# Performance work log

Hardware: AMD Instinct MI355X
Metric: run time of the kernel (lower is better)

Reference implementation:

```python
import jax, jax.numpy as jnp
import numpy as np

SPATIAL, CROP = 128, 256


def definePsf(N, M, slope):
    # standard LCT psf (O'Toole et al.), as used in Wenzheng Chen's torch port
    x = (np.arange(2 * N, dtype=np.float32) / (2 * N - 1)) * 2 - 1
    z = (np.arange(2 * M, dtype=np.float32) / (2 * M - 1)) * 2
    gy, gx = np.meshgrid(x, x)
    psf = np.abs(((4 * slope) ** 2) * (gx[None] ** 2 + gy[None] ** 2) - z[:, None, None])
    psf = (psf == psf.min(axis=0, keepdims=True)).astype(np.float32)
    psf = psf / psf[:, N, N].sum()
    psf = psf / np.linalg.norm(psf.ravel())
    psf = np.roll(psf, N, axis=1)
    psf = np.roll(psf, N, axis=2)
    return psf


def resamplingOperator(M):
    row = M ** 2
    x = np.arange(row, dtype=np.float64) + 1
    mtx = np.zeros((row, M), dtype=np.float64)
    mtx[np.arange(row), (np.ceil(np.sqrt(x)) - 1).astype(np.int64)] = 1
    mtx = mtx / x[:, None]
    mtxi = mtx.T.copy()
    for _ in range(int(np.log2(M))):
        mtx = 0.5 * (mtx[0::2] + mtx[1::2])
        mtxi = 0.5 * (mtxi[:, 0::2] + mtxi[:, 1::2])
    return mtx.astype(np.float32), mtxi.astype(np.float32)


def setup_inputs() -> dict:
    key = jax.random.key(0)
    k1, k2 = jax.random.split(key)
    B, D, T, H = 1, 1, CROP, SPATIAL
    feture = jax.random.uniform(k1, (B, D, T, H, H), dtype=jnp.float32)

    c = 3e8
    bin_len = 0.01
    wall_size = 2.0
    trange = CROP * c * (bin_len / c)
    slope = (wall_size / 2.0) / trange
    psf = definePsf(SPATIAL, CROP, slope)
    fpsf = np.fft.fftn(psf)
    snr = 0.1
    invpsf = np.conjugate(fpsf) / (1.0 / snr + np.real(fpsf) ** 2 + np.imag(fpsf) ** 2)

    mtx, mtxi = resamplingOperator(CROP)
    gridz = (np.arange(CROP, dtype=np.float32) / (CROP - 1)).reshape(1, CROP, 1, 1)
    learnable_w = 0.01 * jax.random.normal(k2, (2,) + psf.shape, dtype=jnp.float32)

    return dict(
        feture=feture,
        gridz=jnp.asarray(gridz),
        mtx=jnp.asarray(mtx),
        mtxi=jnp.asarray(mtxi),
        invpsf_real=jnp.asarray(np.real(invpsf).astype(np.float32)),
        invpsf_imag=jnp.asarray(np.imag(invpsf).astype(np.float32)),
        learnable_w=learnable_w,
    )


def reference(feture, gridz, mtx, mtxi, invpsf_real, invpsf_imag, learnable_w):
    B, D, T, H, W = feture.shape
    # diffuse falloff compensation: * z^4
    data = feture.reshape(B * D, T, H, W) * gridz ** 4
    # temporal resampling GEMM: [M,T] @ [BD,T,HW]
    tmp = jnp.einsum('mt,bthw->bmhw', mtx, data)
    # zero-pad to 2T x 2H x 2W
    pad = jnp.zeros((B * D, 2 * T, 2 * H, 2 * W), jnp.float32).at[:, :T, :H, :W].set(tmp)
    # full (non-onesided) complex 3D FFT of real data
    fre = jnp.fft.fftn(pad, axes=(1, 2, 3))
    # learned + fixed inverse filter in frequency domain
    wf = (learnable_w[0] + invpsf_real) + 1j * (learnable_w[1] + invpsf_imag)
    vol = jnp.fft.ifftn(fre * wf, axes=(1, 2, 3)).real[:, :T, :H, :W]
    # inverse temporal resampling GEMM
    out = jnp.einsum('mt,bthw->bmhw', mtxi, vol)
    return out.reshape(B, D, T, H, W)
```

## Files before the change

### kernel.cpp

```cpp
#include <hip/hip_runtime.h>
#include <math.h>

#define TC 256
#define HC 128
#define Z2 512
#define Y2 256
#define X2 256
#define HW 16384
#define LSTR256 260
#define LSTR512 519
#define WPAD 132
#define KZS 257

__device__ __forceinline__ float2 cadd(float2 a, float2 b){ return make_float2(a.x+b.x, a.y+b.y); }
__device__ __forceinline__ float2 csub(float2 a, float2 b){ return make_float2(a.x-b.x, a.y-b.y); }

template<int SGN>
__device__ __forceinline__ float2 cmul_tw(float2 z, float2 w){
  float wy = (SGN < 0) ? w.y : -w.y;
  return make_float2(z.x*w.x - z.y*wy, z.x*wy + z.y*w.x);
}
template<int SGN>
__device__ __forceinline__ float2 mul_pmi(float2 t){
  return (SGN < 0) ? make_float2(t.y, -t.x) : make_float2(-t.y, t.x);
}

template<int SGN>
__device__ __forceinline__ void dft16(float2 r[16], const float2* __restrict__ tw){
  float2 u[16];
  #pragma unroll
  for (int b2=0;b2<4;b2++){
    float2 x0=r[b2], x1=r[4+b2], x2=r[8+b2], x3=r[12+b2];
    float2 t0=cadd(x0,x2), t1=csub(x0,x2), t2=cadd(x1,x3), t3=csub(x1,x3);
    float2 y0=cadd(t0,t2), y2=csub(t0,t2);
    float2 t3i = mul_pmi<SGN>(t3);
    float2 y1=cadd(t1,t3i), y3=csub(t1,t3i);
    u[0*4+b2]=y0;
    u[1*4+b2]=cmul_tw<SGN>(y1, tw[(16*b2)&255]);
    u[2*4+b2]=cmul_tw<SGN>(y2, tw[(32*b2)&255]);
    u[3*4+b2]=cmul_tw<SGN>(y3, tw[(48*b2)&255]);
  }
  #pragma unroll
  for (int e2=0;e2<4;e2++){
    float2 x0=u[e2*4+0], x1=u[e2*4+1], x2=u[e2*4+2], x3=u[e2*4+3];
    float2 t0=cadd(x0,x2), t1=csub(x0,x2), t2=cadd(x1,x3), t3=csub(x1,x3);
    float2 t3i = mul_pmi<SGN>(t3);
    r[0*4+e2]=cadd(t0,t2);
    r[1*4+e2]=cadd(t1,t3i);
    r[2*4+e2]=csub(t0,t2);
    r[3*4+e2]=csub(t1,t3i);
  }
}

template<int SGN>
__device__ __forceinline__ void fft256_reg(float2 r[16], float2* ln, int b,
                                           const float2* __restrict__ tw){
  dft16<SGN>(r, tw);
  #pragma unroll
  for (int e=1;e<16;e++) r[e] = cmul_tw<SGN>(r[e], tw[(b*e)&255]);
  #pragma unroll
  for (int e=0;e<16;e++) ln[16*e+b] = r[e];
  __syncthreads();
  #pragma unroll
  for (int a=0;a<16;a++) r[a] = ln[16*b+a];
  dft16<SGN>(r, tw);
}

template<int SGN>
__device__ __forceinline__ void fft256(float2* ln, int b, const float2* __restrict__ tw){
  float2 r[16];
  #pragma unroll
  for (int a=0;a<16;a++) r[a] = ln[16*a+b];
  dft16<SGN>(r, tw);
  #pragma unroll
  for (int e=1;e<16;e++) r[e] = cmul_tw<SGN>(r[e], tw[(b*e)&255]);
  __syncthreads();
  #pragma unroll
  for (int e=0;e<16;e++) ln[16*e+b] = r[e];
  __syncthreads();
  #pragma unroll
  for (int a=0;a<16;a++) r[a] = ln[16*b+a];
  dft16<SGN>(r, tw);
  __syncthreads();
  #pragma unroll
  for (int d=0;d<16;d++) ln[16*d+b] = r[d];
  __syncthreads();
}

template<int SGN, bool HALF_IN>
__device__ __forceinline__ void fft512_reg(float2* ln, int lt,
        const float2* __restrict__ tw256, const float2* __restrict__ tw512,
        float2 res[8], float2& x256){
  int team = lt >> 4, b = lt & 15;
  float2* sc = ln + team*256;
  float2 r[16];
  #pragma unroll
  for (int a=0;a<16;a++){
    if (HALF_IN && a>=8) r[a] = make_float2(0.f,0.f);
    else r[a] = ln[2*(16*a+b) + team];
  }
  dft16<SGN>(r, tw256);
  #pragma unroll
  for (int e=1;e<16;e++) r[e] = cmul_tw<SGN>(r[e], tw256[(b*e)&255]);
  __syncthreads();
  #pragma unroll
  for (int e=0;e<16;e++) sc[16*e+b] = r[e];
  __syncthreads();
  #pragma unroll
  for (int a=0;a<16;a++) r[a] = sc[16*b+a];
  dft16<SGN>(r, tw256);
  __syncthreads();
  if (team==0){
    #pragma unroll
    for (int d=0;d<16;d++) ln[16*d+b] = r[d];
  } else {
    #pragma unroll
    for (int d=0;d<16;d++){ int k=16*d+b; ln[256+k] = cmul_tw<SGN>(r[d], tw512[k]); }
  }
  __syncthreads();
  #pragma unroll
  for (int j=0;j<8;j++){
    int k = lt + 32*j;
    float2 E = ln[k], WO = ln[256+k];
    res[j] = cadd(E,WO);
    if (j==0) x256 = csub(E,WO);
  }
}

__global__ void k_init_tw(float2* tw256, float2* tw512){
  int j = threadIdx.x;
  if (j < 512){
    double a = -6.283185307179586476925286766559 * (double)j / 512.0;
    tw512[j] = make_float2((float)cos(a), (float)sin(a));
  }
  if (j < 256){
    double a = -6.283185307179586476925286766559 * (double)j / 256.0;
    tw256[j] = make_float2((float)cos(a), (float)sin(a));
  }
}

__global__ __launch_bounds__(256) void k_gemm(const float* __restrict__ A,
    const float* __restrict__ Bv, const float* __restrict__ gz, float* __restrict__ C){
  __shared__ float As[64][8];
  __shared__ float zz[256];
  int tid = threadIdx.x;
  int hw0 = blockIdx.x*1024 + tid*4;
  int m0 = blockIdx.y*8;
  float4 acc[8];
  #pragma unroll
  for (int i=0;i<8;i++) acc[i]=make_float4(0.f,0.f,0.f,0.f);
  {
    float s = 1.f;
    if (gz){ float g = gz[tid]; float g2=g*g; s = g2*g2; }
    zz[tid] = s;
  }
  for (int t0=0;t0<256;t0+=64){
    __syncthreads();
    #pragma unroll
    for (int e=0;e<2;e++){
      int idx = e*256 + tid;
      int tt = idx >> 3, mi = idx & 7;
      As[tt][mi] = A[(size_t)(m0+mi)*256 + t0 + tt] * zz[t0+tt];
    }
    __syncthreads();
    for (int ts=0;ts<64;ts+=8){
      float4 v[8];
      #pragma unroll
      for (int j=0;j<8;j++) v[j] = *(const float4*)(Bv + (size_t)(t0+ts+j)*HW + hw0);
      #pragma unroll
      for (int j=0;j<8;j++){
        const float4* row = (const float4*)&As[ts+j][0];
        float4 alo = row[0], ahi = row[1];
        acc[0].x += alo.x*v[j].x; acc[0].y += alo.x*v[j].y; acc[0].z += alo.x*v[j].z; acc[0].w += alo.x*v[j].w;
        acc[1].x += alo.y*v[j].x; acc[1].y += alo.y*v[j].y; acc[1].z += alo.y*v[j].z; acc[1].w += alo.y*v[j].w;
        acc[2].x += alo.z*v[j].x; acc[2].y += alo.z*v[j].y; acc[2].z += alo.z*v[j].z; acc[2].w += alo.z*v[j].w;
        acc[3].x += alo.w*v[j].x; acc[3].y += alo.w*v[j].y; acc[3].z += alo.w*v[j].z; acc[3].w += alo.w*v[j].w;
        acc[4].x += ahi.x*v[j].x; acc[4].y += ahi.x*v[j].y; acc[4].z += ahi.x*v[j].z; acc[4].w += ahi.x*v[j].w;
        acc[5].x += ahi.y*v[j].x; acc[5].y += ahi.y*v[j].y; acc[5].z += ahi.y*v[j].z; acc[5].w += ahi.y*v[j].w;
        acc[6].x += ahi.z*v[j].x; acc[6].y += ahi.z*v[j].y; acc[6].z += ahi.z*v[j].z; acc[6].w += ahi.z*v[j].w;
        acc[7].x += ahi.w*v[j].x; acc[7].y += ahi.w*v[j].y; acc[7].z += ahi.w*v[j].z; acc[7].w += ahi.w*v[j].w;
      }
    }
  }
  #pragma unroll
  for (int mi=0;mi<8;mi++) *(float4*)(C + (size_t)(m0+mi)*HW + hw0) = acc[mi];
}

__global__ __launch_bounds__(512) void k_fft_zf(const float* __restrict__ tmp,
      float2* __restrict__ A, const float2* __restrict__ tw256, const float2* __restrict__ tw512){
  __shared__ float2 buf[16*LSTR512];
  int tid = threadIdx.x;
  int hwl = tid & 15, ng = tid >> 4;
  int hw = blockIdx.x*16 + hwl;
  size_t colbase = (size_t)(hw>>7)*WPAD + (hw & 127);
  float2* ln = buf + hwl*LSTR512;
  #pragma unroll
  for (int a=0;a<8;a++){
    int n = a*32 + ng;
    ln[n] = make_float2(tmp[(size_t)n*HW + hw], 0.f);
  }
  __syncthreads();
  float2 res[8], x256;
  fft512_reg<-1,true>(ln, ng, tw256, tw512, res, x256);
  #pragma unroll
  for (int j=0;j<8;j++){
    int n = ng + 32*j;
    A[(size_t)n*(128*WPAD) + colbase] = res[j];
  }
  if (ng==0) A[(size_t)256*(128*WPAD) + colbase] = x256;
}

__global__ __launch_bounds__(256) void k_fft_yf(const float2* __restrict__ A,
      float2* __restrict__ B, const float2* __restrict__ tw256){
  __shared__ float2 buf[16*LSTR256];
  int tid = threadIdx.x;
  int w = tid & 15, b = tid >> 4;
  int kz = blockIdx.x;
  int wx = blockIdx.y*16 + w;
  float2* ln = buf + w*LSTR256;
  size_t abase = (size_t)kz*(128*WPAD) + wx;
  float2 r[16];
  #pragma unroll
  for (int a=0;a<8;a++) r[a] = A[abase + (size_t)(16*a+b)*WPAD];
  #pragma unroll
  for (int a=8;a<16;a++) r[a] = make_float2(0.f,0.f);
  fft256_reg<-1>(r, ln, b, tw256);
  size_t bbase = (size_t)kz*(256*WPAD) + wx;
  #pragma unroll
  for (int a=0;a<16;a++) B[bbase + (size_t)(16*a+b)*WPAD] = r[a];
}

__global__ __launch_bounds__(256) void k_x_filt(float2* __restrict__ B,
      const float* __restrict__ R, const float* __restrict__ I,
      const float* __restrict__ w0, const float* __restrict__ w1,
      const float2* __restrict__ tw256){
  __shared__ float2 buf[16*LSTR256];
  const float sc = 1.f/33554432.f;
  int tid = threadIdx.x;
  int wl = tid >> 4, b = tid & 15;
  int kz = blockIdx.y;
  int ky = blockIdx.x*16 + wl;
  float2* ln = buf + wl*LSTR256;
  size_t rb = ((size_t)kz*256 + ky)*WPAD;
  #pragma unroll
  for (int a=0;a<8;a++){
    int n = 16*a + b;
    ln[n] = B[rb + n];
    ln[n+128] = make_float2(0.f,0.f);
  }
  __syncthreads();
  fft256<-1>(ln, b, tw256);
  unsigned mz = (512u - (unsigned)kz) & 511u;
  unsigned my = (256u - (unsigned)ky) & 255u;
  size_t trow = ((size_t)kz<<16) + (size_t)ky*256;
  size_t mrow = ((size_t)mz<<16) + (size_t)my*256;
  const float* Rrow  = R  + trow;
  const float* Irow  = I  + trow;
  const float* w0row = w0 + trow;
  const float* w1row = w1 + trow;
  const float* w0mr  = w0 + mrow;
  const float* w1mr  = w1 + mrow;
  #pragma unroll
  for (int L=0; L<4; ++L){
    int k0 = L*64 + 4*b;
    float4 Rf  = *(const float4*)(Rrow  + k0);
    float4 If  = *(const float4*)(Irow  + k0);
    float4 w0f = *(const float4*)(w0row + k0);
    float4 w1f = *(const float4*)(w1row + k0);
    float4 q0 = *(const float4*)(w0mr + 252 - k0);
    float4 q1 = *(const float4*)(w1mr + 252 - k0);
    float s0 = w0mr[(256 - k0) & 255];
    float s1 = w1mr[(256 - k0) & 255];
    float w0m0=s0, w0m1=q0.w, w0m2=q0.z, w0m3=q0.y;
    float w1m0=s1, w1m1=q1.w, w1m2=q1.z, w1m3=q1.y;
    float wr0=(Rf.x+0.5f*(w0f.x+w0m0))*sc, wi0=(If.x+0.5f*(w1f.x-w1m0))*sc;
    float wr1=(Rf.y+0.5f*(w0f.y+w0m1))*sc, wi1=(If.y+0.5f*(w1f.y-w1m1))*sc;
    float wr2=(Rf.z+0.5f*(w0f.z+w0m2))*sc, wi2=(If.z+0.5f*(w1f.z-w1m2))*sc;
    float wr3=(Rf.w+0.5f*(w0f.w+w0m3))*sc, wi3=(If.w+0.5f*(w1f.w-w1m3))*sc;
    float2 v0=ln[k0], v1=ln[k0+1], v2=ln[k0+2], v3=ln[k0+3];
    ln[k0]   = make_float2(v0.x*wr0 - v0.y*wi0, v0.x*wi0 + v0.y*wr0);
    ln[k0+1] = make_float2(v1.x*wr1 - v1.y*wi1, v1.x*wi1 + v1.y*wr1);
    ln[k0+2] = make_float2(v2.x*wr2 - v2.y*wi2, v2.x*wi2 + v2.y*wr2);
    ln[k0+3] = make_float2(v3.x*wr3 - v3.y*wi3, v3.x*wi3 + v3.y*wr3);
  }
  __syncthreads();
  fft256<1>(ln, b, tw256);
  #pragma unroll
  for (int a=0;a<8;a++){
    int n = 16*a + b;
    B[rb + n] = ln[n];
  }
}

__global__ __launch_bounds__(256) void k_fft_yi(const float2* __restrict__ B,
      float2* __restrict__ A, const float2* __restrict__ tw256){
  __shared__ float2 buf[16*LSTR256];
  int tid = threadIdx.x;
  int w = tid & 15, b = tid >> 4;
  int kz = blockIdx.x;
  int wx = blockIdx.y*16 + w;
  float2* ln = buf + w*LSTR256;
  size_t bbase = (size_t)kz*(256*WPAD) + wx;
  float2 r[16];
  #pragma unroll
  for (int a=0;a<16;a++) r[a] = B[bbase + (size_t)(16*a+b)*WPAD];
  fft256_reg<1>(r, ln, b, tw256);
  size_t abase = (size_t)kz*(128*WPAD) + wx;
  #pragma unroll
  for (int a=0;a<8;a++) A[abase + (size_t)(16*a+b)*WPAD] = r[a];
}

__global__ __launch_bounds__(512) void k_fft_zi(const float2* __restrict__ A,
      float* __restrict__ vol, const float2* __restrict__ tw256, const float2* __restrict__ tw512){
  __shared__ float2 buf[16*LSTR512];
  int tid = threadIdx.x;
  int hwl = tid & 15, ng = tid >> 4;
  int hw = blockIdx.x*16 + hwl;
  size_t colbase = (size_t)(hw>>7)*WPAD + (hw & 127);
  float2* ln = buf + hwl*LSTR512;
  #pragma unroll
  for (int a=0;a<8;a++){
    int n = a*32 + ng;
    ln[n] = A[(size_t)n*(128*WPAD) + colbase];
  }
  if (ng==0) ln[256] = A[(size_t)256*(128*WPAD) + colbase];
  __syncthreads();
  #pragma unroll
  for (int a=8;a<16;a++){
    int n = a*32 + ng;
    if (n > 256){ float2 v = ln[512-n]; ln[n] = make_float2(v.x, -v.y); }
  }
  __syncthreads();
  float2 res[8], dummy;
  fft512_reg<1,false>(ln, ng, tw256, tw512, res, dummy);
  #pragma unroll
  for (int j=0;j<8;j++){
    int n = ng + 32*j;
    vol[(size_t)n*HW + hw] = res[j].x;
  }
}

extern "C" void kernel_launch(void* const* d_in, const int* in_sizes, int n_in,
                              void* d_out, int out_size, void* d_ws, size_t ws_size,
                              hipStream_t stream) {
  const float* fet = (const float*)d_in[0];
  const float* gz  = (const float*)d_in[1];
  const float* mtx = (const float*)d_in[2];
  const float* mtxi= (const float*)d_in[3];
  const float* Rr  = (const float*)d_in[4];
  const float* Ii  = (const float*)d_in[5];
  const float* lw  = (const float*)d_in[6];
  const float* w0  = lw;
  const float* w1  = lw + (size_t)Z2*Y2*X2;
  float* out = (float*)d_out;

  char* ws = (char*)d_ws;
  const size_t OFF_TW256 = 0;
  const size_t OFF_TW512 = 2048;
  const size_t OFF_TMP   = 8192;
  const size_t TMP_BYTES = (size_t)TC*HW*sizeof(float);
  const size_t OFF_A     = OFF_TMP + TMP_BYTES;
  const size_t A_BYTES   = (size_t)KZS*128*WPAD*sizeof(float2);
  const size_t OFF_B     = OFF_A + A_BYTES;
  const size_t B_BYTES   = (size_t)KZS*256*WPAD*sizeof(float2);
  const size_t NEED      = OFF_B + B_BYTES;
  if (ws_size < NEED) return;

  float2* tw256 = (float2*)(ws + OFF_TW256);
  float2* tw512 = (float2*)(ws + OFF_TW512);
  float*  tmp   = (float*)(ws + OFF_TMP);
  float*  vol   = (float*)(ws + OFF_TMP);
  float2* A     = (float2*)(ws + OFF_A);
  float2* B     = (float2*)(ws + OFF_B);

  hipLaunchKernelGGL(k_init_tw, dim3(1), dim3(512), 0, stream, tw256, tw512);
  hipLaunchKernelGGL(k_gemm, dim3(16,32), dim3(256), 0, stream, mtx, fet, gz, tmp);
  hipLaunchKernelGGL(k_fft_zf, dim3(1024), dim3(512), 0, stream, tmp, A, tw256, tw512);
  hipLaunchKernelGGL(k_fft_yf, dim3(KZS,8), dim3(256), 0, stream, A, B, tw256);
  hipLaunchKernelGGL(k_x_filt, dim3(16,KZS), dim3(256), 0, stream, B, Rr, Ii, w0, w1, tw256);
  hipLaunchKernelGGL(k_fft_yi, dim3(KZS,8), dim3(256), 0, stream, B, A, tw256);
  hipLaunchKernelGGL(k_fft_zi, dim3(1024), dim3(512), 0, stream, A, vol, tw256, tw512);
  hipLaunchKernelGGL(k_gemm, dim3(16,32), dim3(256), 0, stream, mtxi, vol, (const float*)nullptr, out);
}
```

Before: 286.0 us.

## Fuse temporal resampling GEMMs into the z-axis FFT kernels

Result: slower. 393.0 us (+37.4%).

```diff
diff --git a/kernel.cpp b/kernel.cpp
--- a/kernel.cpp
+++ b/kernel.cpp
@@ -11,6 +11,7 @@
 #define LSTR512 519
 #define WPAD 132
 #define KZS 257
+#define VSTR 17
 
 __device__ __forceinline__ float2 cadd(float2 a, float2 b){ return make_float2(a.x+b.x, a.y+b.y); }
 __device__ __forceinline__ float2 csub(float2 a, float2 b){ return make_float2(a.x-b.x, a.y-b.y); }
@@ -139,67 +140,41 @@
   }
 }
 
-__global__ __launch_bounds__(256) void k_gemm(const float* __restrict__ A,
-    const float* __restrict__ Bv, const float* __restrict__ gz, float* __restrict__ C){
-  __shared__ float As[64][8];
+__global__ __launch_bounds__(512) void k_zf_gemm(const float* __restrict__ mtxg,
+      const float* __restrict__ fet, const float* __restrict__ gz,
+      float2* __restrict__ A, const float2* __restrict__ tw256, const float2* __restrict__ tw512){
+  __shared__ float2 buf[16*LSTR512];
   __shared__ float zz[256];
   int tid = threadIdx.x;
-  int hw0 = blockIdx.x*1024 + tid*4;
-  int m0 = blockIdx.y*8;
-  float4 acc[8];
-  #pragma unroll
-  for (int i=0;i<8;i++) acc[i]=make_float4(0.f,0.f,0.f,0.f);
+  int hwbase = blockIdx.x*16;
+  if (tid < 256){ float g = gz[tid]; float g2 = g*g; zz[tid] = g2*g2; }
+  __syncthreads();
   {
-    float s = 1.f;
-    if (gz){ float g = gz[tid]; float g2=g*g; s = g2*g2; }
-    zz[tid] = s;
-  }
-  for (int t0=0;t0<256;t0+=64){
-    __syncthreads();
-    #pragma unroll
-    for (int e=0;e<2;e++){
-      int idx = e*256 + tid;
-      int tt = idx >> 3, mi = idx & 7;
-      As[tt][mi] = A[(size_t)(m0+mi)*256 + t0 + tt] * zz[t0+tt];
-    }
-    __syncthreads();
-    for (int ts=0;ts<64;ts+=8){
-      float4 v[8];
-      #pragma unroll
-      for (int j=0;j<8;j++) v[j] = *(const float4*)(Bv + (size_t)(t0+ts+j)*HW + hw0);
+    int c = tid & 15, g = tid >> 4;
+    int hw = hwbase + c;
+    float acc[8];
+    #pragma unroll
+    for (int j=0;j<8;j++) acc[j]=0.f;
+    for (int t0=0;t0<256;t0+=4){
+      float v0 = fet[(size_t)(t0+0)*HW + hw] * zz[t0+0];
+      float v1 = fet[(size_t)(t0+1)*HW + hw] * zz[t0+1];
+      float v2 = fet[(size_t)(t0+2)*HW + hw] * zz[t0+2];
+      float v3 = fet[(size_t)(t0+3)*HW + hw] * zz[t0+3];
       #pragma unroll
       for (int j=0;j<8;j++){
-        const float4* row = (const float4*)&As[ts+j][0];
-        float4 alo = row[0], ahi = row[1];
-        acc[0].x += alo.x*v[j].x; acc[0].y += alo.x*v[j].y; acc[0].z += alo.x*v[j].z; acc[0].w += alo.x*v[j].w;
-        acc[1].x += alo.y*v[j].x; acc[1].y += alo.y*v[j].y; acc[1].z += alo.y*v[j].z; acc[1].w += alo.y*v[j].w;
-        acc[2].x += alo.z*v[j].x; acc[2].y += alo.z*v[j].y; acc[2].z += alo.z*v[j].z; acc[2].w += alo.z*v[j].w;
-        acc[3].x += alo.w*v[j].x; acc[3].y += alo.w*v[j].y; acc[3].z += alo.w*v[j].z; acc[3].w += alo.w*v[j].w;
-        acc[4].x += ahi.x*v[j].x; acc[4].y += ahi.x*v[j].y; acc[4].z += ahi.x*v[j].z; acc[4].w += ahi.x*v[j].w;
-        acc[5].x += ahi.y*v[j].x; acc[5].y += ahi.y*v[j].y; acc[5].z += ahi.y*v[j].z; acc[5].w += ahi.y*v[j].w;
-        acc[6].x += ahi.z*v[j].x; acc[6].y += ahi.z*v[j].y; acc[6].z += ahi.z*v[j].z; acc[6].w += ahi.z*v[j].w;
-        acc[7].x += ahi.w*v[j].x; acc[7].y += ahi.w*v[j].y; acc[7].z += ahi.w*v[j].z; acc[7].w += ahi.w*v[j].w;
+        float4 m4 = *(const float4*)(mtxg + (size_t)(g+32*j)*256 + t0);
+        acc[j] += m4.x*v0 + m4.y*v1 + m4.z*v2 + m4.w*v3;
       }
     }
-  }
-  #pragma unroll
-  for (int mi=0;mi<8;mi++) *(float4*)(C + (size_t)(m0+mi)*HW + hw0) = acc[mi];
-}
-
-__global__ __launch_bounds__(512) void k_fft_zf(const float* __restrict__ tmp,
-      float2* __restrict__ A, const float2* __restrict__ tw256, const float2* __restrict__ tw512){
-  __shared__ float2 buf[16*LSTR512];
-  int tid = threadIdx.x;
+    float2* lnw = buf + c*LSTR512;
+    #pragma unroll
+    for (int j=0;j<8;j++) lnw[g + 32*j] = make_float2(acc[j], 0.f);
+  }
+  __syncthreads();
   int hwl = tid & 15, ng = tid >> 4;
-  int hw = blockIdx.x*16 + hwl;
+  int hw = hwbase + hwl;
   size_t colbase = (size_t)(hw>>7)*WPAD + (hw & 127);
   float2* ln = buf + hwl*LSTR512;
-  #pragma unroll
-  for (int a=0;a<8;a++){
-    int n = a*32 + ng;
-    ln[n] = make_float2(tmp[(size_t)n*HW + hw], 0.f);
-  }
-  __syncthreads();
   float2 res[8], x256;
   fft512_reg<-1,true>(ln, ng, tw256, tw512, res, x256);
   #pragma unroll
@@ -310,12 +285,15 @@
   for (int a=0;a<8;a++) A[abase + (size_t)(16*a+b)*WPAD] = r[a];
 }
 
-__global__ __launch_bounds__(512) void k_fft_zi(const float2* __restrict__ A,
-      float* __restrict__ vol, const float2* __restrict__ tw256, const float2* __restrict__ tw512){
+__global__ __launch_bounds__(512) void k_zi_gemm(const float2* __restrict__ A,
+      const float* __restrict__ mtxig, float* __restrict__ out,
+      const float2* __restrict__ tw256, const float2* __restrict__ tw512){
   __shared__ float2 buf[16*LSTR512];
-  int tid = threadIdx.x;
+  float* vlds = (float*)buf;
+  int tid = threadIdx.x;
+  int hwbase = blockIdx.x*16;
   int hwl = tid & 15, ng = tid >> 4;
-  int hw = blockIdx.x*16 + hwl;
+  int hw = hwbase + hwl;
   size_t colbase = (size_t)(hw>>7)*WPAD + (hw & 127);
   float2* ln = buf + hwl*LSTR512;
   #pragma unroll
@@ -333,10 +311,32 @@
   __syncthreads();
   float2 res[8], dummy;
   fft512_reg<1,false>(ln, ng, tw256, tw512, res, dummy);
+  __syncthreads();
   #pragma unroll
   for (int j=0;j<8;j++){
-    int n = ng + 32*j;
-    vol[(size_t)n*HW + hw] = res[j].x;
+    int t = ng + 32*j;
+    vlds[t*VSTR + hwl] = res[j].x;
+  }
+  __syncthreads();
+  int c2 = tid & 7, g = tid >> 3;
+  float acc0[4] = {0.f,0.f,0.f,0.f};
+  float acc1[4] = {0.f,0.f,0.f,0.f};
+  for (int t0=0;t0<256;t0+=4){
+    float a0 = vlds[(t0+0)*VSTR + 2*c2], b0 = vlds[(t0+0)*VSTR + 2*c2+1];
+    float a1 = vlds[(t0+1)*VSTR + 2*c2], b1 = vlds[(t0+1)*VSTR + 2*c2+1];
+    float a2 = vlds[(t0+2)*VSTR + 2*c2], b2 = vlds[(t0+2)*VSTR + 2*c2+1];
+    float a3 = vlds[(t0+3)*VSTR + 2*c2], b3 = vlds[(t0+3)*VSTR + 2*c2+1];
+    #pragma unroll
+    for (int i=0;i<4;i++){
+      float4 m4 = *(const float4*)(mtxig + (size_t)(g+64*i)*256 + t0);
+      acc0[i] += m4.x*a0 + m4.y*a1 + m4.z*a2 + m4.w*a3;
+      acc1[i] += m4.x*b0 + m4.y*b1 + m4.z*b2 + m4.w*b3;
+    }
+  }
+  #pragma unroll
+  for (int i=0;i<4;i++){
+    int m = g + 64*i;
+    *(float2*)(out + (size_t)m*HW + hwbase + 2*c2) = make_float2(acc0[i], acc1[i]);
   }
 }
 
@@ -357,9 +357,7 @@
   char* ws = (char*)d_ws;
   const size_t OFF_TW256 = 0;
   const size_t OFF_TW512 = 2048;
-  const size_t OFF_TMP   = 8192;
-  const size_t TMP_BYTES = (size_t)TC*HW*sizeof(float);
-  const size_t OFF_A     = OFF_TMP + TMP_BYTES;
+  const size_t OFF_A     = 8192;
   const size_t A_BYTES   = (size_t)KZS*128*WPAD*sizeof(float2);
   const size_t OFF_B     = OFF_A + A_BYTES;
   const size_t B_BYTES   = (size_t)KZS*256*WPAD*sizeof(float2);
@@ -368,17 +366,13 @@
 
   float2* tw256 = (float2*)(ws + OFF_TW256);
   float2* tw512 = (float2*)(ws + OFF_TW512);
-  float*  tmp   = (float*)(ws + OFF_TMP);
-  float*  vol   = (float*)(ws + OFF_TMP);
   float2* A     = (float2*)(ws + OFF_A);
   float2* B     = (float2*)(ws + OFF_B);
 
   hipLaunchKernelGGL(k_init_tw, dim3(1), dim3(512), 0, stream, tw256, tw512);
-  hipLaunchKernelGGL(k_gemm, dim3(16,32), dim3(256), 0, stream, mtx, fet, gz, tmp);
-  hipLaunchKernelGGL(k_fft_zf, dim3(1024), dim3(512), 0, stream, tmp, A, tw256, tw512);
+  hipLaunchKernelGGL(k_zf_gemm, dim3(1024), dim3(512), 0, stream, mtx, fet, gz, A, tw256, tw512);
   hipLaunchKernelGGL(k_fft_yf, dim3(KZS,8), dim3(256), 0, stream, A, B, tw256);
   hipLaunchKernelGGL(k_x_filt, dim3(16,KZS), dim3(256), 0, stream, B, Rr, Ii, w0, w1, tw256);
   hipLaunchKernelGGL(k_fft_yi, dim3(KZS,8), dim3(256), 0, stream, B, A, tw256);
-  hipLaunchKernelGGL(k_fft_zi, dim3(1024), dim3(512), 0, stream, A, vol, tw256, tw512);
-  hipLaunchKernelGGL(k_gemm, dim3(16,32), dim3(256), 0, stream, mtxi, vol, (const float*)nullptr, out);
-}
+  hipLaunchKernelGGL(k_zi_gemm, dim3(1024), dim3(512), 0, stream, A, mtxi, out, tw256, tw512);
+}
```
